# Optimization experiments

Hardware: AMD Instinct MI355X
Metric: run time of the kernel (lower is better)

Reference implementation:

```python
import jax, jax.numpy as jnp
from jax import lax
import numpy as np

# Model dims (match init_kwargs / MolDecoder defaults)
V, E, H, Z, L, T = 64, 64, 256, 128, 3, 120
B = 4096


def _uinit(k, shape, fan):
    # PyTorch-style uniform(-1/sqrt(fan), 1/sqrt(fan)) init
    bound = 1.0 / np.sqrt(fan).astype(np.float32)
    return jax.random.uniform(k, shape, jnp.float32, -bound, bound)


def setup_inputs() -> dict:
    key = jax.random.key(0)
    ks = jax.random.split(key, 32)
    inp = {
        'z': jax.random.normal(ks[0], (B, Z), jnp.float32),
        # nn.Embedding with padding_idx=0 -> row 0 is zeros
        'emb': jax.random.normal(ks[1], (V, E), jnp.float32).at[0].set(0.0),
        'z2h_w': _uinit(ks[2], (H * L, Z), Z),
        'z2h_b': _uinit(ks[3], (H * L,), Z),
        'out_w': _uinit(ks[4], (V, H), H),
        'out_b': _uinit(ks[5], (V,), H),
    }
    kidx = 6
    for l in range(L):
        din = E if l == 0 else H
        inp[f'w_ih_{l}'] = _uinit(ks[kidx + 0], (3 * H, din), H)
        inp[f'w_hh_{l}'] = _uinit(ks[kidx + 1], (3 * H, H), H)
        inp[f'b_ih_{l}'] = _uinit(ks[kidx + 2], (3 * H,), H)
        inp[f'b_hh_{l}'] = _uinit(ks[kidx + 3], (3 * H,), H)
        kidx += 4
    return inp


def _gru_cell(x, h, wi, wh, bi, bh):
    # PyTorch GRUCell math
    gi = x @ wi.T + bi            # [B, 3H]
    gh = h @ wh.T + bh            # [B, 3H]
    ir, iz, inn = jnp.split(gi, 3, axis=-1)
    hr, hz, hn = jnp.split(gh, 3, axis=-1)
    r = jax.nn.sigmoid(ir + hr)
    u = jax.nn.sigmoid(iz + hz)
    n = jnp.tanh(inn + r * hn)
    return (1.0 - u) * n + u * h


def reference(z, emb, z2h_w, z2h_b, out_w, out_b,
              w_ih_0, w_hh_0, b_ih_0, b_hh_0,
              w_ih_1, w_hh_1, b_ih_1, b_hh_1,
              w_ih_2, w_hh_2, b_ih_2, b_hh_2):
    batch = z.shape[0]
    layers = [(w_ih_0, w_hh_0, b_ih_0, b_hh_0),
              (w_ih_1, w_hh_1, b_ih_1, b_hh_1),
              (w_ih_2, w_hh_2, b_ih_2, b_hh_2)]
    # z -> initial hidden [L, B, H]
    h0 = jnp.tanh(z @ z2h_w.T + z2h_b).reshape(batch, L, H).transpose(1, 0, 2)
    tok0 = jnp.ones((batch,), jnp.int32)  # start token = 1 (torch.ones)

    def step(carry, _):
        h, tok = carry
        x = emb[tok]                       # [B, E]
        new_h = []
        for l, (wi, wh, bi, bh) in enumerate(layers):
            hl = _gru_cell(x, h[l], wi, wh, bi, bh)
            new_h.append(hl)
            x = hl
        logits = x @ out_w.T + out_b       # [B, V]
        next_tok = jnp.argmax(logits, axis=-1).astype(jnp.int32)
        return (jnp.stack(new_h), next_tok), logits

    _, logits_seq = lax.scan(step, (h0, tok0), None, length=T - 1)
    return logits_seq.transpose(1, 0, 2)   # [B, T-1, V]
```

## Files before the change

kernel.cpp:

```cpp
#include <hip/hip_runtime.h>
#include <hip/hip_bf16.h>

typedef __bf16 bf16;
typedef __bf16 bf16x8 __attribute__((ext_vector_type(8)));
typedef float  f32x4  __attribute__((ext_vector_type(4)));

#define MFMA16(a,b,c) __builtin_amdgcn_mfma_f32_16x16x32_bf16((a),(b),(c),0,0,0)
#define NSTEP 119

#define O_L0   0u
#define O_L1   491520u
#define O_L2   1277952u
#define O_Z2H  2064384u
#define O_OUTW 2260992u
#define FH0 1146880u
#define FH1 2195456u
#define FH2 3244032u
#define FTOK 4292608u

#define FOFF(m,k) (((k)>>5)*512 + ((m) + 16*(((k)>>3)&3))*8 + ((k)&7))

__device__ __forceinline__ f32x4 splat4(float v){ f32x4 r={v,v,v,v}; return r; }
__device__ __forceinline__ float sigf(float x){ return 1.f/(1.f+expf(-x)); }

__global__ void pack2(const float* __restrict__ src, bf16* __restrict__ dst,
                      int Rt, int KTm, int KTg, int ktoff, int K) {
  int idx = blockIdx.x * 256 + threadIdx.x;
  if (idx >= Rt * KTm * 64) return;
  int lane = idx & 63, fi = idx >> 6;
  int r15 = lane & 15, q = lane >> 4;
  int c = fi / KTm, ktm = fi - c * KTm;
  const float* s = src + (size_t)(c * 16 + r15) * K + ktm * 32 + q * 8;
  bf16* d = dst + (size_t)(c * KTg + ktoff + ktm) * 1024 + lane * 8;
  #pragma unroll
  for (int e = 0; e < 8; ++e) {
    float v = s[e];
    bf16 hi = (bf16)v;
    d[e] = hi;
    d[e + 512] = (bf16)(v - (float)hi);
  }
}

__global__ __launch_bounds__(512)
void kinit(const float* __restrict__ z, const float* __restrict__ z2h_b,
           const bf16* __restrict__ wsb, float* __restrict__ wsf,
           int* __restrict__ wsi)
{
  __shared__ __align__(16) bf16 zF[2][2048];
  const int tid = threadIdx.x, wv = tid >> 6, lane = tid & 63;
  const int q = lane >> 4, r15 = lane & 15;
  const int b0 = blockIdx.x * 16;
  {
    const int m = tid >> 5, c4 = (tid & 31) * 4;
    float4 v = *(const float4*)(z + (size_t)(b0 + m) * 128 + c4);
    const float vv[4] = {v.x, v.y, v.z, v.w};
    #pragma unroll
    for (int e = 0; e < 4; ++e) {
      int off = FOFF(m, c4 + e);
      bf16 hi = (bf16)vv[e];
      zF[0][off] = hi;
      zF[1][off] = (bf16)(vv[e] - (float)hi);
    }
    if (tid < 16) wsi[FTOK + b0 + tid] = 1;
  }
  __syncthreads();
  f32x4 acc[6];
  #pragma unroll
  for (int t = 0; t < 6; ++t) acc[t] = splat4(z2h_b[(wv * 6 + t) * 16 + r15]);
  #pragma unroll
  for (int kt = 0; kt < 4; ++kt) {
    bf16x8 a0 = *(const bf16x8*)(&zF[0][kt * 512 + lane * 8]);
    bf16x8 a1 = *(const bf16x8*)(&zF[1][kt * 512 + lane * 8]);
    #pragma unroll
    for (int t = 0; t < 6; ++t) {
      const bf16* bb = wsb + O_Z2H + (size_t)((wv * 6 + t) * 4 + kt) * 1024 + lane * 8;
      bf16x8 b0 = *(const bf16x8*)bb;
      bf16x8 b1 = *(const bf16x8*)(bb + 512);
      acc[t] = MFMA16(a0, b0, acc[t]);
      acc[t] = MFMA16(a1, b0, acc[t]);
      acc[t] = MFMA16(a0, b1, acc[t]);
    }
  }
  #pragma unroll
  for (int t = 0; t < 6; ++t) {
    const int col = (wv * 6 + t) * 16 + r15;
    const int lay = col >> 8, j = col & 255;
    float* H = wsf + (lay == 0 ? FH0 : lay == 1 ? FH1 : FH2);
    #pragma unroll
    for (int r = 0; r < 4; ++r)
      H[(size_t)(b0 + q * 4 + r) * 256 + j] = tanhf(acc[t][r]);
  }
}

__device__ __forceinline__ void gl16(bf16x8& d, const bf16* p) {
  asm volatile("global_load_dwordx4 %0, %1, off" : "=v"(d) : "v"(p));
}

template<int L, int KTI, int KTG>
__global__ __launch_bounds__(512)
void klayer(const float* __restrict__ emb,
            const float* __restrict__ bih, const float* __restrict__ bhh,
            const float* __restrict__ out_b,
            const bf16* __restrict__ wsb, float* __restrict__ wsf,
            int* __restrict__ wsi, float* __restrict__ out, int step)
{
  constexpr int KT = KTI + 8;
  __shared__ __align__(16) bf16 AiF[2][KTI * 512];
  __shared__ __align__(16) bf16 AhF[2][8 * 512];
  __shared__ float logS2[2][16][68];
  const int tid = threadIdx.x, wv = tid >> 6, lane = tid & 63;
  const int q = lane >> 4, r15 = lane & 15;
  const int b0 = blockIdx.x * 16;
  const size_t WB = (L == 0) ? O_L0 : (L == 1) ? O_L1 : O_L2;
  const unsigned FHcur = (L == 0) ? FH0 : (L == 1) ? FH1 : FH2;

  if constexpr (L == 0) {
    if (tid < 256) {
      const int m = tid >> 4, e4 = (tid & 15) * 4;
      const int tk = wsi[FTOK + b0 + m];
      float4 v = *(const float4*)(emb + (size_t)tk * 64 + e4);
      const float vv[4] = {v.x, v.y, v.z, v.w};
      #pragma unroll
      for (int e = 0; e < 4; ++e) {
        int off = FOFF(m, e4 + e);
        bf16 hi = (bf16)vv[e];
        AiF[0][off] = hi;
        AiF[1][off] = (bf16)(vv[e] - (float)hi);
      }
    }
  } else {
    const unsigned FHin = (L == 1) ? FH0 : FH1;
    const int m = tid >> 5, c8 = (tid & 31) * 8;
    float4 v0 = *(const float4*)(wsf + FHin + (size_t)(b0 + m) * 256 + c8);
    float4 v1 = *(const float4*)(wsf + FHin + (size_t)(b0 + m) * 256 + c8 + 4);
    const float vv[8] = {v0.x, v0.y, v0.z, v0.w, v1.x, v1.y, v1.z, v1.w};
    #pragma unroll
    for (int e = 0; e < 8; ++e) {
      int off = FOFF(m, c8 + e);
      bf16 hi = (bf16)vv[e];
      AiF[0][off] = hi;
      AiF[1][off] = (bf16)(vv[e] - (float)hi);
    }
  }
  {
    const int m = tid >> 5, c8 = (tid & 31) * 8;
    float4 v0 = *(const float4*)(wsf + FHcur + (size_t)(b0 + m) * 256 + c8);
    float4 v1 = *(const float4*)(wsf + FHcur + (size_t)(b0 + m) * 256 + c8 + 4);
    const float vv[8] = {v0.x, v0.y, v0.z, v0.w, v1.x, v1.y, v1.z, v1.w};
    #pragma unroll
    for (int e = 0; e < 8; ++e) {
      int off = FOFF(m, c8 + e);
      bf16 hi = (bf16)vv[e];
      AhF[0][off] = hi;
      AhF[1][off] = (bf16)(vv[e] - (float)hi);
    }
  }
  __syncthreads();

  f32x4 aR[2], aZ[2], aNI[2], aNH[2];
  #pragma unroll
  for (int jt = 0; jt < 2; ++jt) {
    aR[jt] = splat4(0.f); aZ[jt] = splat4(0.f);
    aNI[jt] = splat4(0.f); aNH[jt] = splat4(0.f);
  }
  const bf16* bp[6];
  #pragma unroll
  for (int g3 = 0; g3 < 3; ++g3)
    #pragma unroll
    for (int jt = 0; jt < 2; ++jt)
      bp[g3 * 2 + jt] = wsb + WB + (size_t)((g3 * 16 + wv * 2 + jt) * KTG) * 1024 + lane * 8;

  bf16x8 rb[2][6][2];
  asm volatile("s_waitcnt vmcnt(0)" ::: "memory");
  __builtin_amdgcn_sched_barrier(0);
  #pragma unroll
  for (int t = 0; t < 6; ++t) {
    gl16(rb[0][t][0], bp[t]);
    gl16(rb[0][t][1], bp[t] + 512);
  }
  #pragma unroll
  for (int kt = 0; kt < KT; ++kt) {
    const int s = kt & 1;
    if (kt + 1 < KT) {
      #pragma unroll
      for (int t = 0; t < 6; ++t) {
        gl16(rb[s ^ 1][t][0], bp[t] + (size_t)(kt + 1) * 1024);
        gl16(rb[s ^ 1][t][1], bp[t] + (size_t)(kt + 1) * 1024 + 512);
      }
      asm volatile("s_waitcnt vmcnt(12)" ::: "memory");
    } else {
      asm volatile("s_waitcnt vmcnt(0)" ::: "memory");
    }
    __builtin_amdgcn_sched_barrier(0);
    const bf16* A0;
    const bf16* A1;
    if (kt < KTI) { A0 = &AiF[0][kt * 512]; A1 = &AiF[1][kt * 512]; }
    else          { A0 = &AhF[0][(kt - KTI) * 512]; A1 = &AhF[1][(kt - KTI) * 512]; }
    bf16x8 a0 = *(const bf16x8*)(A0 + lane * 8);
    bf16x8 a1 = *(const bf16x8*)(A1 + lane * 8);
    #pragma unroll
    for (int jt = 0; jt < 2; ++jt) {
      aR[jt] = MFMA16(a0, rb[s][jt][0], aR[jt]);
      aR[jt] = MFMA16(a1, rb[s][jt][0], aR[jt]);
      aR[jt] = MFMA16(a0, rb[s][jt][1], aR[jt]);
      aZ[jt] = MFMA16(a0, rb[s][2 + jt][0], aZ[jt]);
      aZ[jt] = MFMA16(a1, rb[s][2 + jt][0], aZ[jt]);
      aZ[jt] = MFMA16(a0, rb[s][2 + jt][1], aZ[jt]);
      f32x4& aN = (kt < KTI) ? aNI[jt] : aNH[jt];
      aN = MFMA16(a0, rb[s][4 + jt][0], aN);
      aN = MFMA16(a1, rb[s][4 + jt][0], aN);
      aN = MFMA16(a0, rb[s][4 + jt][1], aN);
    }
  }

  float hnew[2][4];
  #pragma unroll
  for (int jt = 0; jt < 2; ++jt) {
    const int j = wv * 32 + jt * 16 + r15;
    const float brz = bih[j] + bhh[j];
    const float bz  = bih[256 + j] + bhh[256 + j];
    const float bni = bih[512 + j];
    const float bnh = bhh[512 + j];
    #pragma unroll
    for (int r = 0; r < 4; ++r) {
      const int m = q * 4 + r;
      float rg = sigf(aR[jt][r] + brz);
      float zg = sigf(aZ[jt][r] + bz);
      float ng = tanhf(aNI[jt][r] + bni + rg * (aNH[jt][r] + bnh));
      float hp = wsf[FHcur + (size_t)(b0 + m) * 256 + j];
      float hv = (1.f - zg) * ng + zg * hp;
      wsf[FHcur + (size_t)(b0 + m) * 256 + j] = hv;
      hnew[jt][r] = hv;
    }
  }

  if constexpr (L == 2) {
    __syncthreads();
    #pragma unroll
    for (int jt = 0; jt < 2; ++jt) {
      const int j = wv * 32 + jt * 16 + r15;
      #pragma unroll
      for (int r = 0; r < 4; ++r) {
        const int off = FOFF(q * 4 + r, j);
        bf16 hi = (bf16)hnew[jt][r];
        AhF[0][off] = hi;
        AhF[1][off] = (bf16)(hnew[jt][r] - (float)hi);
      }
    }
    __syncthreads();
    {
      const int ks = wv >> 2, tt = wv & 3;
      f32x4 acc = ks ? splat4(0.f) : splat4(out_b[tt * 16 + r15]);
      #pragma unroll
      for (int kt2 = 0; kt2 < 4; ++kt2) {
        const int kg = ks * 4 + kt2;
        bf16x8 a0 = *(const bf16x8*)(&AhF[0][kg * 512 + lane * 8]);
        bf16x8 a1 = *(const bf16x8*)(&AhF[1][kg * 512 + lane * 8]);
        const bf16* bb = wsb + O_OUTW + (size_t)(tt * 8 + kg) * 1024 + lane * 8;
        bf16x8 b0 = *(const bf16x8*)bb;
        bf16x8 b1 = *(const bf16x8*)(bb + 512);
        acc = MFMA16(a0, b0, acc);
        acc = MFMA16(a1, b0, acc);
        acc = MFMA16(a0, b1, acc);
      }
      #pragma unroll
      for (int r = 0; r < 4; ++r)
        logS2[ks][q * 4 + r][tt * 16 + r15] = acc[r];
    }
    __syncthreads();
    #pragma unroll
    for (int k2 = 0; k2 < 2; ++k2) {
      const int rr = wv * 2 + k2;
      float v = logS2[0][rr][lane] + logS2[1][rr][lane];
      out[((size_t)(b0 + rr) * NSTEP + step) * 64 + lane] = v;
      float bv = v; int bi = lane;
      #pragma unroll
      for (int d = 1; d < 64; d <<= 1) {
        float ov = __shfl_xor(bv, d);
        int   oi = __shfl_xor(bi, d);
        if (ov > bv || (ov == bv && oi < bi)) { bv = ov; bi = oi; }
      }
      if (lane == 0) wsi[FTOK + b0 + rr] = bi;
    }
  }
}

extern "C" void kernel_launch(void* const* d_in, const int* in_sizes, int n_in,
                              void* d_out, int out_size, void* d_ws, size_t ws_size,
                              hipStream_t stream) {
  bf16*  wsb = (bf16*)d_ws;
  float* wsf = (float*)d_ws;
  int*   wsi = (int*)d_ws;
  const float* z     = (const float*)d_in[0];
  const float* emb   = (const float*)d_in[1];
  const float* z2h_b = (const float*)d_in[3];
  const float* out_b = (const float*)d_in[5];
  const float* bih0 = (const float*)d_in[8],  *bhh0 = (const float*)d_in[9];
  const float* bih1 = (const float*)d_in[12], *bhh1 = (const float*)d_in[13];
  const float* bih2 = (const float*)d_in[16], *bhh2 = (const float*)d_in[17];
  float* out = (float*)d_out;

  pack2<<<24, 256, 0, stream>>>((const float*)d_in[6],  wsb + O_L0,  48, 2, 10, 0, 64);
  pack2<<<96, 256, 0, stream>>>((const float*)d_in[7],  wsb + O_L0,  48, 8, 10, 2, 256);
  pack2<<<96, 256, 0, stream>>>((const float*)d_in[10], wsb + O_L1,  48, 8, 16, 0, 256);
  pack2<<<96, 256, 0, stream>>>((const float*)d_in[11], wsb + O_L1,  48, 8, 16, 8, 256);
  pack2<<<96, 256, 0, stream>>>((const float*)d_in[14], wsb + O_L2,  48, 8, 16, 0, 256);
  pack2<<<96, 256, 0, stream>>>((const float*)d_in[15], wsb + O_L2,  48, 8, 16, 8, 256);
  pack2<<<48, 256, 0, stream>>>((const float*)d_in[2],  wsb + O_Z2H, 48, 4, 4,  0, 128);
  pack2<<<8,  256, 0, stream>>>((const float*)d_in[4],  wsb + O_OUTW, 4, 8, 8,  0, 256);

  kinit<<<256, 512, 0, stream>>>(z, z2h_b, wsb, wsf, wsi);

  for (int t = 0; t < NSTEP; ++t) {
    klayer<0, 2, 10><<<256, 512, 0, stream>>>(emb, bih0, bhh0, out_b, wsb, wsf, wsi, out, t);
    klayer<1, 8, 16><<<256, 512, 0, stream>>>(emb, bih1, bhh1, out_b, wsb, wsf, wsi, out, t);
    klayer<2, 8, 16><<<256, 512, 0, stream>>>(emb, bih2, bhh2, out_b, wsb, wsf, wsi, out, t);
  }
}
```

Before: 6.656 ms.

## Restructure GRU step: stage weight tiles in LDS, split logits, ping-pong hidden states

Each layer kernel now splits work so a block holds one column group for eight row tiles. The block loads that group's weight tiles into shared memory once, and each wave reuses them for its own 16-row tile. Before, every wave streamed its own weight slice from global memory. Hidden states are stored in fragment layout with ping-pong buffers, and the output projection and argmax move to a separate klogits kernel that writes the next embedding directly. This adds a fourth launch per step and uses a large LDS footprint, which may lower occupancy.

```diff
diff --git a/kernel.cpp b/kernel.cpp
--- a/kernel.cpp
+++ b/kernel.cpp
@@ -13,10 +13,13 @@
 #define O_L2   1277952u
 #define O_Z2H  2064384u
 #define O_OUTW 2260992u
-#define FH0 1146880u
-#define FH1 2195456u
-#define FH2 3244032u
-#define FTOK 4292608u
+#define FXF   1146880u
+#define FH0A  1409024u
+#define FH0B  2457600u
+#define FH1A  3506176u
+#define FH1B  4554752u
+#define FH2A  5603328u
+#define FH2B  6651904u
 
 #define FOFF(m,k) (((k)>>5)*512 + ((m) + 16*(((k)>>3)&3))*8 + ((k)&7))
 
@@ -42,14 +45,15 @@
 }
 
 __global__ __launch_bounds__(512)
-void kinit(const float* __restrict__ z, const float* __restrict__ z2h_b,
-           const bf16* __restrict__ wsb, float* __restrict__ wsf,
-           int* __restrict__ wsi)
+void kinit(const float* __restrict__ z, const float* __restrict__ emb,
+           const float* __restrict__ z2h_b, const bf16* __restrict__ wsb,
+           float* __restrict__ xf, float* __restrict__ h0,
+           float* __restrict__ h1, float* __restrict__ h2)
 {
   __shared__ __align__(16) bf16 zF[2][2048];
   const int tid = threadIdx.x, wv = tid >> 6, lane = tid & 63;
   const int q = lane >> 4, r15 = lane & 15;
-  const int b0 = blockIdx.x * 16;
+  const int rt = blockIdx.x, b0 = rt * 16;
   {
     const int m = tid >> 5, c4 = (tid & 31) * 4;
     float4 v = *(const float4*)(z + (size_t)(b0 + m) * 128 + c4);
@@ -61,7 +65,10 @@
       zF[0][off] = hi;
       zF[1][off] = (bf16)(vv[e] - (float)hi);
     }
-    if (tid < 16) wsi[FTOK + b0 + tid] = 1;
+  }
+  for (int i = tid; i < 1024; i += 512) {
+    int m = i >> 6, e = i & 63;
+    xf[(size_t)rt * 1024 + FOFF(m, e)] = emb[64 + e];
   }
   __syncthreads();
   f32x4 acc[6];
@@ -85,138 +92,101 @@
   for (int t = 0; t < 6; ++t) {
     const int col = (wv * 6 + t) * 16 + r15;
     const int lay = col >> 8, j = col & 255;
-    float* H = wsf + (lay == 0 ? FH0 : lay == 1 ? FH1 : FH2);
+    float* H = lay == 0 ? h0 : lay == 1 ? h1 : h2;
     #pragma unroll
     for (int r = 0; r < 4; ++r)
-      H[(size_t)(b0 + q * 4 + r) * 256 + j] = tanhf(acc[t][r]);
-  }
-}
-
-__device__ __forceinline__ void gl16(bf16x8& d, const bf16* p) {
-  asm volatile("global_load_dwordx4 %0, %1, off" : "=v"(d) : "v"(p));
-}
-
-template<int L, int KTI, int KTG>
+      H[(size_t)rt * 4096 + FOFF(q * 4 + r, j)] = tanhf(acc[t][r]);
+  }
+}
+
+template<int L>
 __global__ __launch_bounds__(512)
-void klayer(const float* __restrict__ emb,
-            const float* __restrict__ bih, const float* __restrict__ bhh,
-            const float* __restrict__ out_b,
-            const bf16* __restrict__ wsb, float* __restrict__ wsf,
-            int* __restrict__ wsi, float* __restrict__ out, int step)
+void kgate(const float* __restrict__ ain, const float* __restrict__ hin,
+           float* __restrict__ hout,
+           const float* __restrict__ bih, const float* __restrict__ bhh,
+           const bf16* __restrict__ wsb)
 {
-  constexpr int KT = KTI + 8;
-  __shared__ __align__(16) bf16 AiF[2][KTI * 512];
-  __shared__ __align__(16) bf16 AhF[2][8 * 512];
-  __shared__ float logS2[2][16][68];
+  constexpr int KTI = (L == 0) ? 2 : 8;
+  constexpr int KT  = KTI + 8;
+  constexpr int PH  = (L == 0) ? 10 : 8;
+  constexpr int NPH = (L == 0) ? 1 : 2;
+  constexpr int AST = (L == 0) ? 1024 : 4096;
+  const size_t WB = (L == 0) ? O_L0 : (L == 1) ? O_L1 : O_L2;
+
+  __shared__ __align__(16) bf16 WS[PH][6][1024];
+
   const int tid = threadIdx.x, wv = tid >> 6, lane = tid & 63;
   const int q = lane >> 4, r15 = lane & 15;
-  const int b0 = blockIdx.x * 16;
-  const size_t WB = (L == 0) ? O_L0 : (L == 1) ? O_L1 : O_L2;
-  const unsigned FHcur = (L == 0) ? FH0 : (L == 1) ? FH1 : FH2;
-
-  if constexpr (L == 0) {
-    if (tid < 256) {
-      const int m = tid >> 4, e4 = (tid & 15) * 4;
-      const int tk = wsi[FTOK + b0 + m];
-      float4 v = *(const float4*)(emb + (size_t)tk * 64 + e4);
-      const float vv[4] = {v.x, v.y, v.z, v.w};
+  const int rg = blockIdx.x >> 3, cg = blockIdx.x & 7;
+  const int rt = rg * 8 + wv;
+
+  const float* Ain = ain + (size_t)rt * AST;
+  const float* Ah  = hin + (size_t)rt * 4096;
+
+  f32x4 accR[2], accZ[2], accNI[2], accNH[2];
+  #pragma unroll
+  for (int c = 0; c < 2; ++c) {
+    accR[c] = splat4(0.f); accZ[c] = splat4(0.f);
+    accNI[c] = splat4(0.f); accNH[c] = splat4(0.f);
+  }
+
+  #pragma unroll
+  for (int p = 0; p < NPH; ++p) {
+    const int kb = p * PH;
+    for (int u = wv; u < 6 * PH; u += 8) {
+      int ct = u % 6, ktp = u / 6;
+      int c = (ct >> 1) * 16 + cg * 2 + (ct & 1);
+      const bf16* src = wsb + WB + (size_t)(c * KT + kb + ktp) * 1024 + lane * 8;
+      bf16x8 t0 = *(const bf16x8*)src;
+      bf16x8 t1 = *(const bf16x8*)(src + 512);
+      *(bf16x8*)(&WS[ktp][ct][lane * 8]) = t0;
+      *(bf16x8*)(&WS[ktp][ct][512 + lane * 8]) = t1;
+    }
+    __syncthreads();
+    const float* ap0 = (kb < KTI) ? (Ain + (size_t)kb * 512 + lane * 8)
+                                  : (Ah + (size_t)(kb - KTI) * 512 + lane * 8);
+    float4 va = *(const float4*)ap0;
+    float4 vb = *(const float4*)(ap0 + 4);
+    #pragma unroll
+    for (int ktp = 0; ktp < PH; ++ktp) {
+      const int kt = kb + ktp;
+      float4 na, nb;
+      if (ktp + 1 < PH) {
+        const int kn = kt + 1;
+        const float* apn = (kn < KTI) ? (Ain + (size_t)kn * 512 + lane * 8)
+                                      : (Ah + (size_t)(kn - KTI) * 512 + lane * 8);
+        na = *(const float4*)apn;
+        nb = *(const float4*)(apn + 4);
+      }
+      const float vv[8] = {va.x, va.y, va.z, va.w, vb.x, vb.y, vb.z, vb.w};
+      bf16x8 a0, a1;
       #pragma unroll
-      for (int e = 0; e < 4; ++e) {
-        int off = FOFF(m, e4 + e);
+      for (int e = 0; e < 8; ++e) {
         bf16 hi = (bf16)vv[e];
-        AiF[0][off] = hi;
-        AiF[1][off] = (bf16)(vv[e] - (float)hi);
-      }
-    }
-  } else {
-    const unsigned FHin = (L == 1) ? FH0 : FH1;
-    const int m = tid >> 5, c8 = (tid & 31) * 8;
-    float4 v0 = *(const float4*)(wsf + FHin + (size_t)(b0 + m) * 256 + c8);
-    float4 v1 = *(const float4*)(wsf + FHin + (size_t)(b0 + m) * 256 + c8 + 4);
-    const float vv[8] = {v0.x, v0.y, v0.z, v0.w, v1.x, v1.y, v1.z, v1.w};
-    #pragma unroll
-    for (int e = 0; e < 8; ++e) {
-      int off = FOFF(m, c8 + e);
-      bf16 hi = (bf16)vv[e];
-      AiF[0][off] = hi;
-      AiF[1][off] = (bf16)(vv[e] - (float)hi);
-    }
-  }
-  {
-    const int m = tid >> 5, c8 = (tid & 31) * 8;
-    float4 v0 = *(const float4*)(wsf + FHcur + (size_t)(b0 + m) * 256 + c8);
-    float4 v1 = *(const float4*)(wsf + FHcur + (size_t)(b0 + m) * 256 + c8 + 4);
-    const float vv[8] = {v0.x, v0.y, v0.z, v0.w, v1.x, v1.y, v1.z, v1.w};
-    #pragma unroll
-    for (int e = 0; e < 8; ++e) {
-      int off = FOFF(m, c8 + e);
-      bf16 hi = (bf16)vv[e];
-      AhF[0][off] = hi;
-      AhF[1][off] = (bf16)(vv[e] - (float)hi);
-    }
-  }
-  __syncthreads();
-
-  f32x4 aR[2], aZ[2], aNI[2], aNH[2];
-  #pragma unroll
-  for (int jt = 0; jt < 2; ++jt) {
-    aR[jt] = splat4(0.f); aZ[jt] = splat4(0.f);
-    aNI[jt] = splat4(0.f); aNH[jt] = splat4(0.f);
-  }
-  const bf16* bp[6];
-  #pragma unroll
-  for (int g3 = 0; g3 < 3; ++g3)
-    #pragma unroll
-    for (int jt = 0; jt < 2; ++jt)
-      bp[g3 * 2 + jt] = wsb + WB + (size_t)((g3 * 16 + wv * 2 + jt) * KTG) * 1024 + lane * 8;
-
-  bf16x8 rb[2][6][2];
-  asm volatile("s_waitcnt vmcnt(0)" ::: "memory");
-  __builtin_amdgcn_sched_barrier(0);
-  #pragma unroll
-  for (int t = 0; t < 6; ++t) {
-    gl16(rb[0][t][0], bp[t]);
-    gl16(rb[0][t][1], bp[t] + 512);
-  }
-  #pragma unroll
-  for (int kt = 0; kt < KT; ++kt) {
-    const int s = kt & 1;
-    if (kt + 1 < KT) {
+        a0[e] = hi;
+        a1[e] = (bf16)(vv[e] - (float)hi);
+      }
       #pragma unroll
-      for (int t = 0; t < 6; ++t) {
-        gl16(rb[s ^ 1][t][0], bp[t] + (size_t)(kt + 1) * 1024);
-        gl16(rb[s ^ 1][t][1], bp[t] + (size_t)(kt + 1) * 1024 + 512);
-      }
-      asm volatile("s_waitcnt vmcnt(12)" ::: "memory");
-    } else {
-      asm volatile("s_waitcnt vmcnt(0)" ::: "memory");
-    }
-    __builtin_amdgcn_sched_barrier(0);
-    const bf16* A0;
-    const bf16* A1;
-    if (kt < KTI) { A0 = &AiF[0][kt * 512]; A1 = &AiF[1][kt * 512]; }
-    else          { A0 = &AhF[0][(kt - KTI) * 512]; A1 = &AhF[1][(kt - KTI) * 512]; }
-    bf16x8 a0 = *(const bf16x8*)(A0 + lane * 8);
-    bf16x8 a1 = *(const bf16x8*)(A1 + lane * 8);
-    #pragma unroll
-    for (int jt = 0; jt < 2; ++jt) {
-      aR[jt] = MFMA16(a0, rb[s][jt][0], aR[jt]);
-      aR[jt] = MFMA16(a1, rb[s][jt][0], aR[jt]);
-      aR[jt] = MFMA16(a0, rb[s][jt][1], aR[jt]);
-      aZ[jt] = MFMA16(a0, rb[s][2 + jt][0], aZ[jt]);
-      aZ[jt] = MFMA16(a1, rb[s][2 + jt][0], aZ[jt]);
-      aZ[jt] = MFMA16(a0, rb[s][2 + jt][1], aZ[jt]);
-      f32x4& aN = (kt < KTI) ? aNI[jt] : aNH[jt];
-      aN = MFMA16(a0, rb[s][4 + jt][0], aN);
-      aN = MFMA16(a1, rb[s][4 + jt][0], aN);
-      aN = MFMA16(a0, rb[s][4 + jt][1], aN);
-    }
-  }
-
-  float hnew[2][4];
-  #pragma unroll
-  for (int jt = 0; jt < 2; ++jt) {
-    const int j = wv * 32 + jt * 16 + r15;
+      for (int ct = 0; ct < 6; ++ct) {
+        bf16x8 b0 = *(const bf16x8*)(&WS[ktp][ct][lane * 8]);
+        bf16x8 b1 = *(const bf16x8*)(&WS[ktp][ct][512 + lane * 8]);
+        f32x4* acc;
+        const int ctl = ct & 1;
+        if (ct < 2)      acc = &accR[ctl];
+        else if (ct < 4) acc = &accZ[ctl];
+        else             acc = (kt < KTI) ? &accNI[ctl] : &accNH[ctl];
+        *acc = MFMA16(a0, b0, *acc);
+        *acc = MFMA16(a1, b0, *acc);
+        *acc = MFMA16(a0, b1, *acc);
+      }
+      va = na; vb = nb;
+    }
+    if (p + 1 < NPH) __syncthreads();
+  }
+
+  #pragma unroll
+  for (int ctl = 0; ctl < 2; ++ctl) {
+    const int j = cg * 32 + ctl * 16 + r15;
     const float brz = bih[j] + bhh[j];
     const float bz  = bih[256 + j] + bhh[256 + j];
     const float bni = bih[512 + j];
@@ -224,64 +194,68 @@
     #pragma unroll
     for (int r = 0; r < 4; ++r) {
       const int m = q * 4 + r;
-      float rg = sigf(aR[jt][r] + brz);
-      float zg = sigf(aZ[jt][r] + bz);
-      float ng = tanhf(aNI[jt][r] + bni + rg * (aNH[jt][r] + bnh));
-      float hp = wsf[FHcur + (size_t)(b0 + m) * 256 + j];
-      float hv = (1.f - zg) * ng + zg * hp;
-      wsf[FHcur + (size_t)(b0 + m) * 256 + j] = hv;
-      hnew[jt][r] = hv;
-    }
-  }
-
-  if constexpr (L == 2) {
-    __syncthreads();
-    #pragma unroll
-    for (int jt = 0; jt < 2; ++jt) {
-      const int j = wv * 32 + jt * 16 + r15;
+      const size_t idx = (size_t)rt * 4096 + FOFF(m, j);
+      float rg_ = sigf(accR[ctl][r] + brz);
+      float zg  = sigf(accZ[ctl][r] + bz);
+      float ng  = tanhf(accNI[ctl][r] + bni + rg_ * (accNH[ctl][r] + bnh));
+      float hp  = hin[idx];
+      hout[idx] = (1.f - zg) * ng + zg * hp;
+    }
+  }
+}
+
+__global__ __launch_bounds__(512)
+void klogits(const float* __restrict__ h2, float* __restrict__ xf,
+             const float* __restrict__ emb, const float* __restrict__ out_b,
+             const bf16* __restrict__ wsb, float* __restrict__ out, int step)
+{
+  __shared__ float logS2[2][16][68];
+  const int tid = threadIdx.x, wv = tid >> 6, lane = tid & 63;
+  const int q = lane >> 4, r15 = lane & 15;
+  const int rt = blockIdx.x;
+  const float* A = h2 + (size_t)rt * 4096;
+
+  {
+    const int ks = wv >> 2, tt = wv & 3;
+    f32x4 acc = ks ? splat4(0.f) : splat4(out_b[tt * 16 + r15]);
+    #pragma unroll
+    for (int kt2 = 0; kt2 < 4; ++kt2) {
+      const int kg = ks * 4 + kt2;
+      float4 v0 = *(const float4*)(A + kg * 512 + lane * 8);
+      float4 v1 = *(const float4*)(A + kg * 512 + lane * 8 + 4);
+      const float vv[8] = {v0.x, v0.y, v0.z, v0.w, v1.x, v1.y, v1.z, v1.w};
+      bf16x8 a0, a1;
       #pragma unroll
-      for (int r = 0; r < 4; ++r) {
-        const int off = FOFF(q * 4 + r, j);
-        bf16 hi = (bf16)hnew[jt][r];
-        AhF[0][off] = hi;
-        AhF[1][off] = (bf16)(hnew[jt][r] - (float)hi);
-      }
-    }
-    __syncthreads();
-    {
-      const int ks = wv >> 2, tt = wv & 3;
-      f32x4 acc = ks ? splat4(0.f) : splat4(out_b[tt * 16 + r15]);
-      #pragma unroll
-      for (int kt2 = 0; kt2 < 4; ++kt2) {
-        const int kg = ks * 4 + kt2;
-        bf16x8 a0 = *(const bf16x8*)(&AhF[0][kg * 512 + lane * 8]);
-        bf16x8 a1 = *(const bf16x8*)(&AhF[1][kg * 512 + lane * 8]);
-        const bf16* bb = wsb + O_OUTW + (size_t)(tt * 8 + kg) * 1024 + lane * 8;
-        bf16x8 b0 = *(const bf16x8*)bb;
-        bf16x8 b1 = *(const bf16x8*)(bb + 512);
-        acc = MFMA16(a0, b0, acc);
-        acc = MFMA16(a1, b0, acc);
-        acc = MFMA16(a0, b1, acc);
-      }
-      #pragma unroll
-      for (int r = 0; r < 4; ++r)
-        logS2[ks][q * 4 + r][tt * 16 + r15] = acc[r];
-    }
-    __syncthreads();
-    #pragma unroll
-    for (int k2 = 0; k2 < 2; ++k2) {
-      const int rr = wv * 2 + k2;
-      float v = logS2[0][rr][lane] + logS2[1][rr][lane];
-      out[((size_t)(b0 + rr) * NSTEP + step) * 64 + lane] = v;
-      float bv = v; int bi = lane;
-      #pragma unroll
-      for (int d = 1; d < 64; d <<= 1) {
-        float ov = __shfl_xor(bv, d);
-        int   oi = __shfl_xor(bi, d);
-        if (ov > bv || (ov == bv && oi < bi)) { bv = ov; bi = oi; }
-      }
-      if (lane == 0) wsi[FTOK + b0 + rr] = bi;
-    }
+      for (int e = 0; e < 8; ++e) {
+        bf16 hi = (bf16)vv[e];
+        a0[e] = hi;
+        a1[e] = (bf16)(vv[e] - (float)hi);
+      }
+      const bf16* bb = wsb + O_OUTW + (size_t)(tt * 8 + kg) * 1024 + lane * 8;
+      bf16x8 b0 = *(const bf16x8*)bb;
+      bf16x8 b1 = *(const bf16x8*)(bb + 512);
+      acc = MFMA16(a0, b0, acc);
+      acc = MFMA16(a1, b0, acc);
+      acc = MFMA16(a0, b1, acc);
+    }
+    #pragma unroll
+    for (int r = 0; r < 4; ++r)
+      logS2[ks][q * 4 + r][tt * 16 + r15] = acc[r];
+  }
+  __syncthreads();
+  #pragma unroll
+  for (int k2 = 0; k2 < 2; ++k2) {
+    const int rr = wv * 2 + k2;
+    float v = logS2[0][rr][lane] + logS2[1][rr][lane];
+    out[((size_t)(rt * 16 + rr) * NSTEP + step) * 64 + lane] = v;
+    float bv = v; int bi = lane;
+    #pragma unroll
+    for (int d = 1; d < 64; d <<= 1) {
+      float ov = __shfl_xor(bv, d);
+      int   oi = __shfl_xor(bi, d);
+      if (ov > bv || (ov == bv && oi < bi)) { bv = ov; bi = oi; }
+    }
+    xf[(size_t)rt * 1024 + FOFF(rr, lane)] = emb[(size_t)bi * 64 + lane];
   }
 }
 
@@ -290,7 +264,6 @@
                               hipStream_t stream) {
   bf16*  wsb = (bf16*)d_ws;
   float* wsf = (float*)d_ws;
-  int*   wsi = (int*)d_ws;
   const float* z     = (const float*)d_in[0];
   const float* emb   = (const float*)d_in[1];
   const float* z2h_b = (const float*)d_in[3];
@@ -300,6 +273,11 @@
   const float* bih2 = (const float*)d_in[16], *bhh2 = (const float*)d_in[17];
   float* out = (float*)d_out;
 
+  float* xf    = wsf + FXF;
+  float* h0[2] = {wsf + FH0A, wsf + FH0B};
+  float* h1[2] = {wsf + FH1A, wsf + FH1B};
+  float* h2[2] = {wsf + FH2A, wsf + FH2B};
+
   pack2<<<24, 256, 0, stream>>>((const float*)d_in[6],  wsb + O_L0,  48, 2, 10, 0, 64);
   pack2<<<96, 256, 0, stream>>>((const float*)d_in[7],  wsb + O_L0,  48, 8, 10, 2, 256);
   pack2<<<96, 256, 0, stream>>>((const float*)d_in[10], wsb + O_L1,  48, 8, 16, 0, 256);
@@ -309,11 +287,13 @@
   pack2<<<48, 256, 0, stream>>>((const float*)d_in[2],  wsb + O_Z2H, 48, 4, 4,  0, 128);
   pack2<<<8,  256, 0, stream>>>((const float*)d_in[4],  wsb + O_OUTW, 4, 8, 8,  0, 256);
 
-  kinit<<<256, 512, 0, stream>>>(z, z2h_b, wsb, wsf, wsi);
+  kinit<<<256, 512, 0, stream>>>(z, emb, z2h_b, wsb, xf, h0[0], h1[0], h2[0]);
 
   for (int t = 0; t < NSTEP; ++t) {
-    klayer<0, 2, 10><<<256, 512, 0, stream>>>(emb, bih0, bhh0, out_b, wsb, wsf, wsi, out, t);
-    klayer<1, 8, 16><<<256, 512, 0, stream>>>(emb, bih1, bhh1, out_b, wsb, wsf, wsi, out, t);
-    klayer<2, 8, 16><<<256, 512, 0, stream>>>(emb, bih2, bhh2, out_b, wsb, wsf, wsi, out, t);
-  }
-}
+    const int p = t & 1, pn = p ^ 1;
+    kgate<0><<<256, 512, 0, stream>>>(xf,     h0[p], h0[pn], bih0, bhh0, wsb);
+    kgate<1><<<256, 512, 0, stream>>>(h0[pn], h1[p], h1[pn], bih1, bhh1, wsb);
+    kgate<2><<<256, 512, 0, stream>>>(h1[pn], h2[p], h2[pn], bih2, bhh2, wsb);
+    klogits<<<256, 512, 0, stream>>>(h2[pn], xf, emb, out_b, wsb, out, t);
+  }
+}
```

Result: no change. 6.596 ms (-0.9%).

## Fuse three per-layer GRU kernels into one per-step kernel

Applied to the files above, without the earlier changes.

Merges the three layer kernels of each time step into a single kernel. Each layer's new hidden state is written straight into shared memory as the split bf16 A operand for the next layer, so it is no longer reloaded from global memory. This cuts launches from 357 to 119 and removes the global round trips of layer outputs. Shared memory per block grows to about 40KB, which may reduce occupancy, and the blocks now run their layers serially with more __syncthreads.

```diff
diff --git a/kernel.cpp b/kernel.cpp
--- a/kernel.cpp
+++ b/kernel.cpp
@@ -96,66 +96,17 @@
   asm volatile("global_load_dwordx4 %0, %1, off" : "=v"(d) : "v"(p));
 }
 
-template<int L, int KTI, int KTG>
-__global__ __launch_bounds__(512)
-void klayer(const float* __restrict__ emb,
-            const float* __restrict__ bih, const float* __restrict__ bhh,
-            const float* __restrict__ out_b,
-            const bf16* __restrict__ wsb, float* __restrict__ wsf,
-            int* __restrict__ wsi, float* __restrict__ out, int step)
+template<int KTI>
+__device__ __forceinline__ void gate_layer(
+    const bf16* __restrict__ Ain0, const bf16* __restrict__ Ain1,
+    const bf16* __restrict__ Ah0,  const bf16* __restrict__ Ah1,
+    bf16* __restrict__ Bout0, bf16* __restrict__ Bout1,
+    const float* __restrict__ bih, const float* __restrict__ bhh,
+    const bf16* __restrict__ Wbase, float* __restrict__ Hg,
+    const int b0, const int wv, const int lane)
 {
   constexpr int KT = KTI + 8;
-  __shared__ __align__(16) bf16 AiF[2][KTI * 512];
-  __shared__ __align__(16) bf16 AhF[2][8 * 512];
-  __shared__ float logS2[2][16][68];
-  const int tid = threadIdx.x, wv = tid >> 6, lane = tid & 63;
   const int q = lane >> 4, r15 = lane & 15;
-  const int b0 = blockIdx.x * 16;
-  const size_t WB = (L == 0) ? O_L0 : (L == 1) ? O_L1 : O_L2;
-  const unsigned FHcur = (L == 0) ? FH0 : (L == 1) ? FH1 : FH2;
-
-  if constexpr (L == 0) {
-    if (tid < 256) {
-      const int m = tid >> 4, e4 = (tid & 15) * 4;
-      const int tk = wsi[FTOK + b0 + m];
-      float4 v = *(const float4*)(emb + (size_t)tk * 64 + e4);
-      const float vv[4] = {v.x, v.y, v.z, v.w};
-      #pragma unroll
-      for (int e = 0; e < 4; ++e) {
-        int off = FOFF(m, e4 + e);
-        bf16 hi = (bf16)vv[e];
-        AiF[0][off] = hi;
-        AiF[1][off] = (bf16)(vv[e] - (float)hi);
-      }
-    }
-  } else {
-    const unsigned FHin = (L == 1) ? FH0 : FH1;
-    const int m = tid >> 5, c8 = (tid & 31) * 8;
-    float4 v0 = *(const float4*)(wsf + FHin + (size_t)(b0 + m) * 256 + c8);
-    float4 v1 = *(const float4*)(wsf + FHin + (size_t)(b0 + m) * 256 + c8 + 4);
-    const float vv[8] = {v0.x, v0.y, v0.z, v0.w, v1.x, v1.y, v1.z, v1.w};
-    #pragma unroll
-    for (int e = 0; e < 8; ++e) {
-      int off = FOFF(m, c8 + e);
-      bf16 hi = (bf16)vv[e];
-      AiF[0][off] = hi;
-      AiF[1][off] = (bf16)(vv[e] - (float)hi);
-    }
-  }
-  {
-    const int m = tid >> 5, c8 = (tid & 31) * 8;
-    float4 v0 = *(const float4*)(wsf + FHcur + (size_t)(b0 + m) * 256 + c8);
-    float4 v1 = *(const float4*)(wsf + FHcur + (size_t)(b0 + m) * 256 + c8 + 4);
-    const float vv[8] = {v0.x, v0.y, v0.z, v0.w, v1.x, v1.y, v1.z, v1.w};
-    #pragma unroll
-    for (int e = 0; e < 8; ++e) {
-      int off = FOFF(m, c8 + e);
-      bf16 hi = (bf16)vv[e];
-      AhF[0][off] = hi;
-      AhF[1][off] = (bf16)(vv[e] - (float)hi);
-    }
-  }
-  __syncthreads();
 
   f32x4 aR[2], aZ[2], aNI[2], aNH[2];
   #pragma unroll
@@ -168,7 +119,7 @@
   for (int g3 = 0; g3 < 3; ++g3)
     #pragma unroll
     for (int jt = 0; jt < 2; ++jt)
-      bp[g3 * 2 + jt] = wsb + WB + (size_t)((g3 * 16 + wv * 2 + jt) * KTG) * 1024 + lane * 8;
+      bp[g3 * 2 + jt] = Wbase + (size_t)((g3 * 16 + wv * 2 + jt) * KT) * 1024 + lane * 8;
 
   bf16x8 rb[2][6][2];
   asm volatile("s_waitcnt vmcnt(0)" ::: "memory");
@@ -194,8 +145,8 @@
     __builtin_amdgcn_sched_barrier(0);
     const bf16* A0;
     const bf16* A1;
-    if (kt < KTI) { A0 = &AiF[0][kt * 512]; A1 = &AiF[1][kt * 512]; }
-    else          { A0 = &AhF[0][(kt - KTI) * 512]; A1 = &AhF[1][(kt - KTI) * 512]; }
+    if (kt < KTI) { A0 = Ain0 + kt * 512; A1 = Ain1 + kt * 512; }
+    else          { A0 = Ah0 + (kt - KTI) * 512; A1 = Ah1 + (kt - KTI) * 512; }
     bf16x8 a0 = *(const bf16x8*)(A0 + lane * 8);
     bf16x8 a1 = *(const bf16x8*)(A1 + lane * 8);
     #pragma unroll
@@ -213,7 +164,6 @@
     }
   }
 
-  float hnew[2][4];
   #pragma unroll
   for (int jt = 0; jt < 2; ++jt) {
     const int j = wv * 32 + jt * 16 + r15;
@@ -227,61 +177,118 @@
       float rg = sigf(aR[jt][r] + brz);
       float zg = sigf(aZ[jt][r] + bz);
       float ng = tanhf(aNI[jt][r] + bni + rg * (aNH[jt][r] + bnh));
-      float hp = wsf[FHcur + (size_t)(b0 + m) * 256 + j];
+      float hp = Hg[(size_t)(b0 + m) * 256 + j];
       float hv = (1.f - zg) * ng + zg * hp;
-      wsf[FHcur + (size_t)(b0 + m) * 256 + j] = hv;
-      hnew[jt][r] = hv;
-    }
-  }
-
-  if constexpr (L == 2) {
-    __syncthreads();
-    #pragma unroll
-    for (int jt = 0; jt < 2; ++jt) {
-      const int j = wv * 32 + jt * 16 + r15;
-      #pragma unroll
-      for (int r = 0; r < 4; ++r) {
-        const int off = FOFF(q * 4 + r, j);
-        bf16 hi = (bf16)hnew[jt][r];
-        AhF[0][off] = hi;
-        AhF[1][off] = (bf16)(hnew[jt][r] - (float)hi);
-      }
-    }
-    __syncthreads();
-    {
-      const int ks = wv >> 2, tt = wv & 3;
-      f32x4 acc = ks ? splat4(0.f) : splat4(out_b[tt * 16 + r15]);
-      #pragma unroll
-      for (int kt2 = 0; kt2 < 4; ++kt2) {
-        const int kg = ks * 4 + kt2;
-        bf16x8 a0 = *(const bf16x8*)(&AhF[0][kg * 512 + lane * 8]);
-        bf16x8 a1 = *(const bf16x8*)(&AhF[1][kg * 512 + lane * 8]);
-        const bf16* bb = wsb + O_OUTW + (size_t)(tt * 8 + kg) * 1024 + lane * 8;
-        bf16x8 b0 = *(const bf16x8*)bb;
-        bf16x8 b1 = *(const bf16x8*)(bb + 512);
-        acc = MFMA16(a0, b0, acc);
-        acc = MFMA16(a1, b0, acc);
-        acc = MFMA16(a0, b1, acc);
-      }
-      #pragma unroll
-      for (int r = 0; r < 4; ++r)
-        logS2[ks][q * 4 + r][tt * 16 + r15] = acc[r];
-    }
-    __syncthreads();
-    #pragma unroll
-    for (int k2 = 0; k2 < 2; ++k2) {
-      const int rr = wv * 2 + k2;
-      float v = logS2[0][rr][lane] + logS2[1][rr][lane];
-      out[((size_t)(b0 + rr) * NSTEP + step) * 64 + lane] = v;
-      float bv = v; int bi = lane;
-      #pragma unroll
-      for (int d = 1; d < 64; d <<= 1) {
-        float ov = __shfl_xor(bv, d);
-        int   oi = __shfl_xor(bi, d);
-        if (ov > bv || (ov == bv && oi < bi)) { bv = ov; bi = oi; }
-      }
-      if (lane == 0) wsi[FTOK + b0 + rr] = bi;
-    }
+      Hg[(size_t)(b0 + m) * 256 + j] = hv;
+      const int off = FOFF(m, j);
+      bf16 hi = (bf16)hv;
+      Bout0[off] = hi;
+      Bout1[off] = (bf16)(hv - (float)hi);
+    }
+  }
+}
+
+__device__ __forceinline__ void stage_h(bf16* __restrict__ B0, bf16* __restrict__ B1,
+                                        const float* __restrict__ Hg, const int b0,
+                                        const int tid)
+{
+  const int m = tid >> 5, c8 = (tid & 31) * 8;
+  float4 v0 = *(const float4*)(Hg + (size_t)(b0 + m) * 256 + c8);
+  float4 v1 = *(const float4*)(Hg + (size_t)(b0 + m) * 256 + c8 + 4);
+  const float vv[8] = {v0.x, v0.y, v0.z, v0.w, v1.x, v1.y, v1.z, v1.w};
+  #pragma unroll
+  for (int e = 0; e < 8; ++e) {
+    int off = FOFF(m, c8 + e);
+    bf16 hi = (bf16)vv[e];
+    B0[off] = hi;
+    B1[off] = (bf16)(vv[e] - (float)hi);
+  }
+}
+
+__global__ __launch_bounds__(512)
+void kstep(const float* __restrict__ emb,
+           const float* __restrict__ bih0, const float* __restrict__ bhh0,
+           const float* __restrict__ bih1, const float* __restrict__ bhh1,
+           const float* __restrict__ bih2, const float* __restrict__ bhh2,
+           const float* __restrict__ out_b,
+           const bf16* __restrict__ wsb, float* __restrict__ wsf,
+           int* __restrict__ wsi, float* __restrict__ out, int step)
+{
+  __shared__ __align__(16) bf16 BxA[2][1024];
+  __shared__ __align__(16) bf16 Bh[2][4096];
+  __shared__ __align__(16) bf16 Bo0[2][4096];
+  __shared__ __align__(16) bf16 Bo1[2][4096];
+  __shared__ float logS2[2][16][68];
+
+  const int tid = threadIdx.x, wv = tid >> 6, lane = tid & 63;
+  const int q = lane >> 4, r15 = lane & 15;
+  const int b0 = blockIdx.x * 16;
+
+  if (tid < 256) {
+    const int m = tid >> 4, e4 = (tid & 15) * 4;
+    const int tk = wsi[FTOK + b0 + m];
+    float4 v = *(const float4*)(emb + (size_t)tk * 64 + e4);
+    const float vv[4] = {v.x, v.y, v.z, v.w};
+    #pragma unroll
+    for (int e = 0; e < 4; ++e) {
+      int off = FOFF(m, e4 + e);
+      bf16 hi = (bf16)vv[e];
+      BxA[0][off] = hi;
+      BxA[1][off] = (bf16)(vv[e] - (float)hi);
+    }
+  }
+  stage_h(Bh[0], Bh[1], wsf + FH0, b0, tid);
+  __syncthreads();
+
+  gate_layer<2>(BxA[0], BxA[1], Bh[0], Bh[1], Bo0[0], Bo0[1],
+                bih0, bhh0, wsb + O_L0, wsf + FH0, b0, wv, lane);
+  __syncthreads();
+  stage_h(Bh[0], Bh[1], wsf + FH1, b0, tid);
+  __syncthreads();
+
+  gate_layer<8>(Bo0[0], Bo0[1], Bh[0], Bh[1], Bo1[0], Bo1[1],
+                bih1, bhh1, wsb + O_L1, wsf + FH1, b0, wv, lane);
+  __syncthreads();
+  stage_h(Bh[0], Bh[1], wsf + FH2, b0, tid);
+  __syncthreads();
+
+  gate_layer<8>(Bo1[0], Bo1[1], Bh[0], Bh[1], Bo0[0], Bo0[1],
+                bih2, bhh2, wsb + O_L2, wsf + FH2, b0, wv, lane);
+  __syncthreads();
+
+  {
+    const int ks = wv >> 2, tt = wv & 3;
+    f32x4 acc = ks ? splat4(0.f) : splat4(out_b[tt * 16 + r15]);
+    #pragma unroll
+    for (int kt2 = 0; kt2 < 4; ++kt2) {
+      const int kg = ks * 4 + kt2;
+      bf16x8 a0 = *(const bf16x8*)(&Bo0[0][kg * 512 + lane * 8]);
+      bf16x8 a1 = *(const bf16x8*)(&Bo0[1][kg * 512 + lane * 8]);
+      const bf16* bb = wsb + O_OUTW + (size_t)(tt * 8 + kg) * 1024 + lane * 8;
+      bf16x8 b0 = *(const bf16x8*)bb;
+      bf16x8 b1 = *(const bf16x8*)(bb + 512);
+      acc = MFMA16(a0, b0, acc);
+      acc = MFMA16(a1, b0, acc);
+      acc = MFMA16(a0, b1, acc);
+    }
+    #pragma unroll
+    for (int r = 0; r < 4; ++r)
+      logS2[ks][q * 4 + r][tt * 16 + r15] = acc[r];
+  }
+  __syncthreads();
+  #pragma unroll
+  for (int k2 = 0; k2 < 2; ++k2) {
+    const int rr = wv * 2 + k2;
+    float v = logS2[0][rr][lane] + logS2[1][rr][lane];
+    out[((size_t)(b0 + rr) * NSTEP + step) * 64 + lane] = v;
+    float bv = v; int bi = lane;
+    #pragma unroll
+    for (int d = 1; d < 64; d <<= 1) {
+      float ov = __shfl_xor(bv, d);
+      int   oi = __shfl_xor(bi, d);
+      if (ov > bv || (ov == bv && oi < bi)) { bv = ov; bi = oi; }
+    }
+    if (lane == 0) wsi[FTOK + b0 + rr] = bi;
   }
 }
 
@@ -311,9 +318,7 @@
 
   kinit<<<256, 512, 0, stream>>>(z, z2h_b, wsb, wsf, wsi);
 
-  for (int t = 0; t < NSTEP; ++t) {
-    klayer<0, 2, 10><<<256, 512, 0, stream>>>(emb, bih0, bhh0, out_b, wsb, wsf, wsi, out, t);
-    klayer<1, 8, 16><<<256, 512, 0, stream>>>(emb, bih1, bhh1, out_b, wsb, wsf, wsi, out, t);
-    klayer<2, 8, 16><<<256, 512, 0, stream>>>(emb, bih2, bhh2, out_b, wsb, wsf, wsi, out, t);
-  }
-}
+  for (int t = 0; t < NSTEP; ++t)
+    kstep<<<256, 512, 0, stream>>>(emb, bih0, bhh0, bih1, bhh1, bih2, bhh2,
+                                   out_b, wsb, wsf, wsi, out, t);
+}
```

New measurement: 6.290 ms. 1.06x faster.
